# Kernel tuning notes

Hardware: AMD Instinct MI355X
Metric: run time of the kernel (lower is better)

The kernel has to match this reference:

```python
import jax, jax.numpy as jnp
import numpy as np

D = 4096          # input_dim == output_dim (square FAUST factors)
N = 1024          # batch rows of U
NNZ = 131072      # nonzeros per factor (32 per row)
K = 4             # number of sparse factors


def setup_inputs() -> dict:
    key = jax.random.key(0)
    k_u, k_b, k_v, k_r, k_c = jax.random.split(key, 5)
    U = jax.random.normal(k_u, (N, D), dtype=jnp.float32)
    bias = jax.random.normal(k_b, (D,), dtype=jnp.float32)
    # glorot-ish scaling: ~32 nnz per row -> scale by 1/sqrt(32) for stable chain
    vals = jax.random.normal(k_v, (K, NNZ), dtype=jnp.float32) * (1.0 / np.sqrt(32.0))
    rows = jax.random.randint(k_r, (K, NNZ), 0, D, dtype=jnp.int32)
    cols = jax.random.randint(k_c, (K, NNZ), 0, D, dtype=jnp.int32)
    return {"U": U, "bias": bias, "vals": vals, "rows": rows, "cols": cols}


def _spmm(rows, cols, vals, X):
    # sparse (COO) [D, D] @ dense X [D, N] -> [D, N]
    return jax.ops.segment_sum(vals[:, None] * X[cols], rows, num_segments=D)


def reference(U, bias, vals, rows, cols):
    # torch code applies sparse_matrices[-1] first, then [k-2] ... [0]
    y = U.T  # [D, N]
    for i in range(K - 1, -1, -1):
        y = _spmm(rows[i], cols[i], vals[i], y)
    return y.T + bias  # [N, D]
```

## Files before the change

### kernel.cpp

```cpp
#include <hip/hip_runtime.h>

#define D_DIM 4096
#define N_DIM 1024
#define NNZ_F 131072
#define K_F 4
#define NCHUNK 8
#define LPR 16
#define RPB 16
#define MAXE 1024
#define XS8 (N_DIM / 8)

#define T_TILES ((D_DIM / 64) * (N_DIM / 64))
#define TSTRIDE 132

__device__ __forceinline__ unsigned short f2bf(float f) {
    union { float f; unsigned int u; } v; v.f = f;
    unsigned int r = v.u + 0x7fffu + ((v.u >> 16) & 1u);
    return (unsigned short)(r >> 16);
}
__device__ __forceinline__ float bf_lo(unsigned int w) {
    return __uint_as_float(w << 16);
}
__device__ __forceinline__ float bf_hi(unsigned int w) {
    return __uint_as_float(w & 0xffff0000u);
}

__global__ __launch_bounds__(1024) void fused_t_build_k(const float* __restrict__ in,
                                                        unsigned short* __restrict__ outb,
                                                        const int* __restrict__ rows,
                                                        int* __restrict__ row_ptr_g,
                                                        int* __restrict__ cursor_g) {
    __shared__ int s_cnt[4 * D_DIM];
    __shared__ int s_part[1024];
    const int tid = threadIdx.x;
    const int bid = blockIdx.x;

    if (bid < T_TILES) {
        float (*tile)[65] = (float (*)[65])s_cnt;
        const int gxi = bid & 63;
        const int gyi = bid >> 6;
        const int c0 = gxi * 64;
        const int r0 = gyi * 64;
        const int tx = tid & 63;
        const int ty = tid >> 6;
#pragma unroll
        for (int i = ty; i < 64; i += 16)
            tile[i][tx] = in[(size_t)(r0 + i) * D_DIM + c0 + tx];
        __syncthreads();
        const int px = (tid & 15) * 4;
        const int py = tid >> 4;
        ushort4 w;
        w.x = f2bf(tile[px + 0][py]);
        w.y = f2bf(tile[px + 1][py]);
        w.z = f2bf(tile[px + 2][py]);
        w.w = f2bf(tile[px + 3][py]);
        *(ushort4*)&outb[(size_t)(c0 + py) * N_DIM + r0 + px] = w;
        return;
    }

    const int f = bid - T_TILES;
    const int grp = (tid >> 8) & 3;
#pragma unroll
    for (int k = 0; k < 16; ++k) s_cnt[tid + k * 1024] = 0;
    __syncthreads();

    int* h = s_cnt + grp * D_DIM;
    const int4* rp4 = (const int4*)(rows + (size_t)f * NNZ_F);
#pragma unroll 4
    for (int it = 0; it < NNZ_F / 4096; ++it) {
        int4 r4 = rp4[(size_t)it * 1024 + tid];
        atomicAdd(&h[r4.x], 1);
        atomicAdd(&h[r4.y], 1);
        atomicAdd(&h[r4.z], 1);
        atomicAdd(&h[r4.w], 1);
    }
    __syncthreads();

    int c[4];
#pragma unroll
    for (int k = 0; k < 4; ++k)
        c[k] = s_cnt[tid * 4 + k] + s_cnt[D_DIM + tid * 4 + k]
             + s_cnt[2 * D_DIM + tid * 4 + k] + s_cnt[3 * D_DIM + tid * 4 + k];
    const int part = c[0] + c[1] + c[2] + c[3];
    s_part[tid] = part;
    __syncthreads();
    for (int off = 1; off < 1024; off <<= 1) {
        int v = (tid >= off) ? s_part[tid - off] : 0;
        __syncthreads();
        s_part[tid] += v;
        __syncthreads();
    }
    int excl = s_part[tid] - part;

    int* rp  = row_ptr_g + (size_t)f * (D_DIM + 1);
    int* cur = cursor_g + (size_t)f * D_DIM;
    int b = tid * 4;
#pragma unroll
    for (int k = 0; k < 4; ++k) {
        rp[b + k] = excl; cur[b + k] = excl; excl += c[k];
    }
    if (tid == 1023) rp[D_DIM] = NNZ_F;
}

__global__ __launch_bounds__(1024) void scatter_all_k(const int* __restrict__ rows,
                                                      const int* __restrict__ cols,
                                                      const float* __restrict__ vals,
                                                      int* __restrict__ cursor,
                                                      int* __restrict__ csr_col,
                                                      float* __restrict__ csr_val) {
    const int f = blockIdx.x >> 7;
    const size_t j = (size_t)(blockIdx.x & 127) * 1024 + threadIdx.x;
    const size_t base = (size_t)f * NNZ_F;
    int r = rows[base + j];
    int p = atomicAdd(&cursor[(size_t)f * D_DIM + r], 1);
    csr_col[base + p] = cols[base + j];
    csr_val[base + p] = vals[base + j];
}

template <bool FINAL>
__global__ __launch_bounds__(256) void spmm_chunk_k(const int* __restrict__ row_ptr,
                                                    const int* __restrict__ csr_col,
                                                    const float* __restrict__ csr_val,
                                                    const uint4* __restrict__ X,
                                                    uint4* __restrict__ Y,
                                                    float* __restrict__ out,
                                                    const float* __restrict__ bias) {
    __shared__ float smem[16 * TSTRIDE];
    int*   s_col = (int*)smem;
    float* s_val = smem + MAXE;
    int*   s_ptr = (int*)(smem + 2 * MAXE);

    const int tid   = threadIdx.x;
    const int chunk = blockIdx.x & (NCHUNK - 1);
    const int rg    = blockIdx.x >> 3;
    const int r0    = rg * RPB;
    const int sub   = tid >> 4;
    const int lane  = tid & 15;
    const int slot  = chunk * LPR + lane;
    const int r     = r0 + sub;

    if (tid <= RPB) s_ptr[tid] = row_ptr[r0 + tid];
    __syncthreads();
    const int base  = s_ptr[0];
    const int total = s_ptr[RPB] - base;
    const int start = s_ptr[sub] - base;
    const int end_  = s_ptr[sub + 1] - base;

    float acc[8];
#pragma unroll
    for (int k = 0; k < 8; ++k) acc[k] = 0.f;

    for (int cb2 = 0; cb2 < total; cb2 += MAXE) {
        int cnt = total - cb2;
        if (cnt > MAXE) cnt = MAXE;
        for (int t = tid; t < cnt; t += 256) {
            s_col[t] = csr_col[base + cb2 + t];
            s_val[t] = csr_val[base + cb2 + t];
        }
        __syncthreads();
        int js = start > cb2 ? start : cb2;
        int je = end_ < cb2 + cnt ? end_ : cb2 + cnt;
        if (js < je) {
            int   jj = js - cb2;
            uint4 x  = X[(size_t)s_col[jj] * XS8 + slot];
            float v  = s_val[jj];
#pragma unroll 2
            for (int j = js + 1; j < je; ++j) {
                const int   jn = j - cb2;
                const uint4 xn = X[(size_t)s_col[jn] * XS8 + slot];
                const float vn = s_val[jn];
                acc[0] += v * bf_lo(x.x);
                acc[1] += v * bf_hi(x.x);
                acc[2] += v * bf_lo(x.y);
                acc[3] += v * bf_hi(x.y);
                acc[4] += v * bf_lo(x.z);
                acc[5] += v * bf_hi(x.z);
                acc[6] += v * bf_lo(x.w);
                acc[7] += v * bf_hi(x.w);
                x = xn; v = vn;
            }
            acc[0] += v * bf_lo(x.x);
            acc[1] += v * bf_hi(x.x);
            acc[2] += v * bf_lo(x.y);
            acc[3] += v * bf_hi(x.y);
            acc[4] += v * bf_lo(x.z);
            acc[5] += v * bf_hi(x.z);
            acc[6] += v * bf_lo(x.w);
            acc[7] += v * bf_hi(x.w);
        }
        __syncthreads();
    }

    if (!FINAL) {
        uint4 o;
        o.x = (unsigned int)f2bf(acc[0]) | ((unsigned int)f2bf(acc[1]) << 16);
        o.y = (unsigned int)f2bf(acc[2]) | ((unsigned int)f2bf(acc[3]) << 16);
        o.z = (unsigned int)f2bf(acc[4]) | ((unsigned int)f2bf(acc[5]) << 16);
        o.w = (unsigned int)f2bf(acc[6]) | ((unsigned int)f2bf(acc[7]) << 16);
        Y[(size_t)r * XS8 + slot] = o;
    } else {
        __syncthreads();
        float* tile = smem;
        const int wbase = sub * TSTRIDE + lane * 8;
        *(float4*)&tile[wbase]     = make_float4(acc[0], acc[1], acc[2], acc[3]);
        *(float4*)&tile[wbase + 4] = make_float4(acc[4], acc[5], acc[6], acc[7]);
        __syncthreads();
        const int n0 = chunk * (N_DIM / NCHUNK);
#pragma unroll
        for (int f = tid; f < 512; f += 256) {
            const int n_loc = f >> 2;
            const int q     = f & 3;
            float4 o;
            o.x = tile[(q * 4 + 0) * TSTRIDE + n_loc];
            o.y = tile[(q * 4 + 1) * TSTRIDE + n_loc];
            o.z = tile[(q * 4 + 2) * TSTRIDE + n_loc];
            o.w = tile[(q * 4 + 3) * TSTRIDE + n_loc];
            const float4 bv = *(const float4*)&bias[r0 + q * 4];
            o.x += bv.x; o.y += bv.y; o.z += bv.z; o.w += bv.w;
            *(float4*)&out[(size_t)(n0 + n_loc) * D_DIM + r0 + q * 4] = o;
        }
    }
}

extern "C" void kernel_launch(void* const* d_in, const int* in_sizes, int n_in,
                              void* d_out, int out_size, void* d_ws, size_t ws_size,
                              hipStream_t stream) {
    const float* U    = (const float*)d_in[0];
    const float* bias = (const float*)d_in[1];
    const float* vals = (const float*)d_in[2];
    const int*   rows = (const int*)d_in[3];
    const int*   cols = (const int*)d_in[4];
    float* out = (float*)d_out;

    char* ws = (char*)d_ws;
    size_t off = 0;
    char* bufA = ws;                   off += (size_t)D_DIM * N_DIM * 2;
    char* bufB = ws + off;             off += (size_t)D_DIM * N_DIM * 2;
    int* row_ptr = (int*)(ws + off);   off += (size_t)K_F * (D_DIM + 1) * 4;
    off = (off + 15) & ~(size_t)15;
    int* cursor  = (int*)(ws + off);   off += (size_t)K_F * D_DIM * 4;
    int*   csr_col = (int*)(ws + off); off += (size_t)K_F * NNZ_F * 4;
    float* csr_val = (float*)(ws + off); off += (size_t)K_F * NNZ_F * 4;

    const int grid_spmm = (D_DIM / RPB) * NCHUNK;

    fused_t_build_k<<<T_TILES + K_F, 1024, 0, stream>>>(
        U, (unsigned short*)bufA, rows, row_ptr, cursor);

    scatter_all_k<<<K_F * (NNZ_F / 1024), 1024, 0, stream>>>(rows, cols, vals, cursor,
                                                             csr_col, csr_val);

    spmm_chunk_k<false><<<grid_spmm, 256, 0, stream>>>(
        row_ptr + 3 * (D_DIM + 1), csr_col + 3 * (size_t)NNZ_F, csr_val + 3 * (size_t)NNZ_F,
        (const uint4*)bufA, (uint4*)bufB, nullptr, nullptr);
    spmm_chunk_k<false><<<grid_spmm, 256, 0, stream>>>(
        row_ptr + 2 * (D_DIM + 1), csr_col + 2 * (size_t)NNZ_F, csr_val + 2 * (size_t)NNZ_F,
        (const uint4*)bufB, (uint4*)bufA, nullptr, nullptr);
    spmm_chunk_k<false><<<grid_spmm, 256, 0, stream>>>(
        row_ptr + 1 * (D_DIM + 1), csr_col + 1 * (size_t)NNZ_F, csr_val + 1 * (size_t)NNZ_F,
        (const uint4*)bufA, (uint4*)bufB, nullptr, nullptr);
    spmm_chunk_k<true><<<grid_spmm, 256, 0, stream>>>(
        row_ptr + 0 * (D_DIM + 1), csr_col + 0 * (size_t)NNZ_F, csr_val + 0 * (size_t)NNZ_F,
        (const uint4*)bufB, nullptr, out, bias);
}
```

Baseline: 113.7 us.

## Pad CSR rows to multiples of four and read indices as int4/float4

Each CSR row is padded to a multiple of four entries with zero values and column 0, so the row pointers stay 16-byte aligned. The SpMM kernel then loads four column indices and four values at once straight from global memory, dropping the shared-memory staging and its block-wide barriers. It also issues four independent X gathers per iteration to expose more memory-level parallelism. In exchange it spends extra work on padded zero entries, uses more workspace, and relies on cache hits for the index reads instead of shared memory.

```diff
diff --git a/kernel.cpp b/kernel.cpp
--- a/kernel.cpp
+++ b/kernel.cpp
@@ -3,11 +3,11 @@
 #define D_DIM 4096
 #define N_DIM 1024
 #define NNZ_F 131072
+#define NNZP (NNZ_F + 3 * D_DIM)
 #define K_F 4
 #define NCHUNK 8
 #define LPR 16
 #define RPB 16
-#define MAXE 1024
 #define XS8 (N_DIM / 8)
 
 #define T_TILES ((D_DIM / 64) * (N_DIM / 64))
@@ -29,7 +29,9 @@
                                                         unsigned short* __restrict__ outb,
                                                         const int* __restrict__ rows,
                                                         int* __restrict__ row_ptr_g,
-                                                        int* __restrict__ cursor_g) {
+                                                        int* __restrict__ cursor_g,
+                                                        int* __restrict__ csr_col_g,
+                                                        float* __restrict__ csr_val_g) {
     __shared__ int s_cnt[4 * D_DIM];
     __shared__ int s_part[1024];
     const int tid = threadIdx.x;
@@ -76,12 +78,15 @@
     }
     __syncthreads();
 
-    int c[4];
-#pragma unroll
-    for (int k = 0; k < 4; ++k)
+    int c[4], plen[4];
+    int part = 0;
+#pragma unroll
+    for (int k = 0; k < 4; ++k) {
         c[k] = s_cnt[tid * 4 + k] + s_cnt[D_DIM + tid * 4 + k]
              + s_cnt[2 * D_DIM + tid * 4 + k] + s_cnt[3 * D_DIM + tid * 4 + k];
-    const int part = c[0] + c[1] + c[2] + c[3];
+        plen[k] = (c[k] + 3) & ~3;
+        part += plen[k];
+    }
     s_part[tid] = part;
     __syncthreads();
     for (int off = 1; off < 1024; off <<= 1) {
@@ -92,14 +97,22 @@
     }
     int excl = s_part[tid] - part;
 
-    int* rp  = row_ptr_g + (size_t)f * (D_DIM + 1);
-    int* cur = cursor_g + (size_t)f * D_DIM;
-    int b = tid * 4;
+    int*   rp  = row_ptr_g + (size_t)f * (D_DIM + 1);
+    int*   cur = cursor_g + (size_t)f * D_DIM;
+    int*   ccol = csr_col_g + (size_t)f * NNZP;
+    float* cval = csr_val_g + (size_t)f * NNZP;
+    const int b = tid * 4;
 #pragma unroll
     for (int k = 0; k < 4; ++k) {
-        rp[b + k] = excl; cur[b + k] = excl; excl += c[k];
-    }
-    if (tid == 1023) rp[D_DIM] = NNZ_F;
+        rp[b + k] = excl;
+        cur[b + k] = excl;
+        for (int p = excl + c[k]; p < excl + plen[k]; ++p) {
+            ccol[p] = 0;
+            cval[p] = 0.f;
+        }
+        excl += plen[k];
+    }
+    if (tid == 1023) rp[D_DIM] = excl;
 }
 
 __global__ __launch_bounds__(1024) void scatter_all_k(const int* __restrict__ rows,
@@ -113,23 +126,19 @@
     const size_t base = (size_t)f * NNZ_F;
     int r = rows[base + j];
     int p = atomicAdd(&cursor[(size_t)f * D_DIM + r], 1);
-    csr_col[base + p] = cols[base + j];
-    csr_val[base + p] = vals[base + j];
+    csr_col[(size_t)f * NNZP + p] = cols[base + j];
+    csr_val[(size_t)f * NNZP + p] = vals[base + j];
 }
 
 template <bool FINAL>
 __global__ __launch_bounds__(256) void spmm_chunk_k(const int* __restrict__ row_ptr,
-                                                    const int* __restrict__ csr_col,
-                                                    const float* __restrict__ csr_val,
+                                                    const int4* __restrict__ col4,
+                                                    const float4* __restrict__ val4,
                                                     const uint4* __restrict__ X,
                                                     uint4* __restrict__ Y,
                                                     float* __restrict__ out,
                                                     const float* __restrict__ bias) {
-    __shared__ float smem[16 * TSTRIDE];
-    int*   s_col = (int*)smem;
-    float* s_val = smem + MAXE;
-    int*   s_ptr = (int*)(smem + 2 * MAXE);
-
+    __shared__ float tile_s[16 * TSTRIDE];
     const int tid   = threadIdx.x;
     const int chunk = blockIdx.x & (NCHUNK - 1);
     const int rg    = blockIdx.x >> 3;
@@ -139,56 +148,41 @@
     const int slot  = chunk * LPR + lane;
     const int r     = r0 + sub;
 
-    if (tid <= RPB) s_ptr[tid] = row_ptr[r0 + tid];
-    __syncthreads();
-    const int base  = s_ptr[0];
-    const int total = s_ptr[RPB] - base;
-    const int start = s_ptr[sub] - base;
-    const int end_  = s_ptr[sub + 1] - base;
+    const int qs = row_ptr[r] >> 2;
+    const int qe = row_ptr[r + 1] >> 2;
 
     float acc[8];
 #pragma unroll
     for (int k = 0; k < 8; ++k) acc[k] = 0.f;
 
-    for (int cb2 = 0; cb2 < total; cb2 += MAXE) {
-        int cnt = total - cb2;
-        if (cnt > MAXE) cnt = MAXE;
-        for (int t = tid; t < cnt; t += 256) {
-            s_col[t] = csr_col[base + cb2 + t];
-            s_val[t] = csr_val[base + cb2 + t];
+    if (qs < qe) {
+        int4   c = col4[qs];
+        float4 v = val4[qs];
+        for (int q = qs + 1; q <= qe; ++q) {
+            const int4   cn = col4[q];
+            const float4 vn = val4[q];
+            const uint4 x0 = X[(size_t)c.x * XS8 + slot];
+            const uint4 x1 = X[(size_t)c.y * XS8 + slot];
+            const uint4 x2 = X[(size_t)c.z * XS8 + slot];
+            const uint4 x3 = X[(size_t)c.w * XS8 + slot];
+            acc[0] += v.x * bf_lo(x0.x); acc[1] += v.x * bf_hi(x0.x);
+            acc[2] += v.x * bf_lo(x0.y); acc[3] += v.x * bf_hi(x0.y);
+            acc[4] += v.x * bf_lo(x0.z); acc[5] += v.x * bf_hi(x0.z);
+            acc[6] += v.x * bf_lo(x0.w); acc[7] += v.x * bf_hi(x0.w);
+            acc[0] += v.y * bf_lo(x1.x); acc[1] += v.y * bf_hi(x1.x);
+            acc[2] += v.y * bf_lo(x1.y); acc[3] += v.y * bf_hi(x1.y);
+            acc[4] += v.y * bf_lo(x1.z); acc[5] += v.y * bf_hi(x1.z);
+            acc[6] += v.y * bf_lo(x1.w); acc[7] += v.y * bf_hi(x1.w);
+            acc[0] += v.z * bf_lo(x2.x); acc[1] += v.z * bf_hi(x2.x);
+            acc[2] += v.z * bf_lo(x2.y); acc[3] += v.z * bf_hi(x2.y);
+            acc[4] += v.z * bf_lo(x2.z); acc[5] += v.z * bf_hi(x2.z);
+            acc[6] += v.z * bf_lo(x2.w); acc[7] += v.z * bf_hi(x2.w);
+            acc[0] += v.w * bf_lo(x3.x); acc[1] += v.w * bf_hi(x3.x);
+            acc[2] += v.w * bf_lo(x3.y); acc[3] += v.w * bf_hi(x3.y);
+            acc[4] += v.w * bf_lo(x3.z); acc[5] += v.w * bf_hi(x3.z);
+            acc[6] += v.w * bf_lo(x3.w); acc[7] += v.w * bf_hi(x3.w);
+            c = cn; v = vn;
         }
-        __syncthreads();
-        int js = start > cb2 ? start : cb2;
-        int je = end_ < cb2 + cnt ? end_ : cb2 + cnt;
-        if (js < je) {
-            int   jj = js - cb2;
-            uint4 x  = X[(size_t)s_col[jj] * XS8 + slot];
-            float v  = s_val[jj];
-#pragma unroll 2
-            for (int j = js + 1; j < je; ++j) {
-                const int   jn = j - cb2;
-                const uint4 xn = X[(size_t)s_col[jn] * XS8 + slot];
-                const float vn = s_val[jn];
-                acc[0] += v * bf_lo(x.x);
-                acc[1] += v * bf_hi(x.x);
-                acc[2] += v * bf_lo(x.y);
-                acc[3] += v * bf_hi(x.y);
-                acc[4] += v * bf_lo(x.z);
-                acc[5] += v * bf_hi(x.z);
-                acc[6] += v * bf_lo(x.w);
-                acc[7] += v * bf_hi(x.w);
-                x = xn; v = vn;
-            }
-            acc[0] += v * bf_lo(x.x);
-            acc[1] += v * bf_hi(x.x);
-            acc[2] += v * bf_lo(x.y);
-            acc[3] += v * bf_hi(x.y);
-            acc[4] += v * bf_lo(x.z);
-            acc[5] += v * bf_hi(x.z);
-            acc[6] += v * bf_lo(x.w);
-            acc[7] += v * bf_hi(x.w);
-        }
-        __syncthreads();
     }
 
     if (!FINAL) {
@@ -199,17 +193,16 @@
         o.w = (unsigned int)f2bf(acc[6]) | ((unsigned int)f2bf(acc[7]) << 16);
         Y[(size_t)r * XS8 + slot] = o;
     } else {
-        __syncthreads();
-        float* tile = smem;
+        float* tile = tile_s;
         const int wbase = sub * TSTRIDE + lane * 8;
         *(float4*)&tile[wbase]     = make_float4(acc[0], acc[1], acc[2], acc[3]);
         *(float4*)&tile[wbase + 4] = make_float4(acc[4], acc[5], acc[6], acc[7]);
         __syncthreads();
         const int n0 = chunk * (N_DIM / NCHUNK);
 #pragma unroll
-        for (int f = tid; f < 512; f += 256) {
-            const int n_loc = f >> 2;
-            const int q     = f & 3;
+        for (int t = tid; t < 512; t += 256) {
+            const int n_loc = t >> 2;
+            const int q     = t & 3;
             float4 o;
             o.x = tile[(q * 4 + 0) * TSTRIDE + n_loc];
             o.y = tile[(q * 4 + 1) * TSTRIDE + n_loc];
@@ -239,27 +232,31 @@
     int* row_ptr = (int*)(ws + off);   off += (size_t)K_F * (D_DIM + 1) * 4;
     off = (off + 15) & ~(size_t)15;
     int* cursor  = (int*)(ws + off);   off += (size_t)K_F * D_DIM * 4;
-    int*   csr_col = (int*)(ws + off); off += (size_t)K_F * NNZ_F * 4;
-    float* csr_val = (float*)(ws + off); off += (size_t)K_F * NNZ_F * 4;
+    int*   csr_col = (int*)(ws + off); off += (size_t)K_F * NNZP * 4 + 16;
+    float* csr_val = (float*)(ws + off); off += (size_t)K_F * NNZP * 4 + 16;
 
     const int grid_spmm = (D_DIM / RPB) * NCHUNK;
 
     fused_t_build_k<<<T_TILES + K_F, 1024, 0, stream>>>(
-        U, (unsigned short*)bufA, rows, row_ptr, cursor);
+        U, (unsigned short*)bufA, rows, row_ptr, cursor, csr_col, csr_val);
 
     scatter_all_k<<<K_F * (NNZ_F / 1024), 1024, 0, stream>>>(rows, cols, vals, cursor,
                                                              csr_col, csr_val);
 
     spmm_chunk_k<false><<<grid_spmm, 256, 0, stream>>>(
-        row_ptr + 3 * (D_DIM + 1), csr_col + 3 * (size_t)NNZ_F, csr_val + 3 * (size_t)NNZ_F,
+        row_ptr + 3 * (D_DIM + 1), (const int4*)(csr_col + 3 * (size_t)NNZP),
+        (const float4*)(csr_val + 3 * (size_t)NNZP),
         (const uint4*)bufA, (uint4*)bufB, nullptr, nullptr);
     spmm_chunk_k<false><<<grid_spmm, 256, 0, stream>>>(
-        row_ptr + 2 * (D_DIM + 1), csr_col + 2 * (size_t)NNZ_F, csr_val + 2 * (size_t)NNZ_F,
+        row_ptr + 2 * (D_DIM + 1), (const int4*)(csr_col + 2 * (size_t)NNZP),
+        (const float4*)(csr_val + 2 * (size_t)NNZP),
         (const uint4*)bufB, (uint4*)bufA, nullptr, nullptr);
     spmm_chunk_k<false><<<grid_spmm, 256, 0, stream>>>(
-        row_ptr + 1 * (D_DIM + 1), csr_col + 1 * (size_t)NNZ_F, csr_val + 1 * (size_t)NNZ_F,
+        row_ptr + 1 * (D_DIM + 1), (const int4*)(csr_col + 1 * (size_t)NNZP),
+        (const float4*)(csr_val + 1 * (size_t)NNZP),
         (const uint4*)bufA, (uint4*)bufB, nullptr, nullptr);
     spmm_chunk_k<true><<<grid_spmm, 256, 0, stream>>>(
-        row_ptr + 0 * (D_DIM + 1), csr_col + 0 * (size_t)NNZ_F, csr_val + 0 * (size_t)NNZ_F,
+        row_ptr + 0 * (D_DIM + 1), (const int4*)(csr_col + 0 * (size_t)NNZP),
+        (const float4*)(csr_val + 0 * (size_t)NNZP),
         (const uint4*)bufB, nullptr, out, bias);
 }
```

After: 129.8 us. 14.2% more time.
